# Kernel tuning notes

Hardware: AMD Instinct MI355X
Metric: run time of the kernel (lower is better)

Reference implementation:

```python
import jax, jax.numpy as jnp
import numpy as np

HEADS = 4
EPS = 1e-5


def _ln(x, g, b):
    m = jnp.mean(x, axis=-1, keepdims=True)
    v = jnp.mean((x - m) ** 2, axis=-1, keepdims=True)
    return (x - m) * jax.lax.rsqrt(v + EPS) * g + b


def _gcn(x, A, W, b):
    # x: [B,N,T,C]; A: [N,N]; W: [C_out, 3C] (1x1 conv); order-2 k-hop propagation
    h = jnp.transpose(x, (0, 3, 1, 2))            # [B,C,N,T]
    h1 = jnp.einsum('bcnt,nm->bcmt', h, A)        # 1-hop
    h2 = jnp.einsum('bcnt,nm->bcmt', h1, A)       # 2-hop
    cat = jnp.concatenate([h, h1, h2], axis=1)    # [B,3C,N,T]
    out = jnp.einsum('bcnt,oc->bont', cat, W) + b[None, :, None, None]
    return jnp.transpose(out, (0, 2, 3, 1))       # [B,N,T,C_out]


def setup_inputs() -> dict:
    key = jax.random.key(0)
    ks = jax.random.split(key, 16)
    B, N, T, H = 8, 2048, 1, 64
    s = 0.02
    return {
        'query': jax.random.normal(ks[0], (B, N, T, H), jnp.float32),
        'adj': jax.random.uniform(ks[1], (N, N), jnp.float32) / N,
        'WF': jax.random.normal(ks[2], (H, 3 * H), jnp.float32) * s,
        'bF': jnp.zeros((H,), jnp.float32),
        'WD': jax.random.normal(ks[3], (H, 3 * H), jnp.float32) * s,
        'bD': jnp.zeros((H,), jnp.float32),
        'ffw1': jax.random.normal(ks[4], (6 * H, H), jnp.float32) * s,
        'ffb1': jnp.zeros((6 * H,), jnp.float32),
        'ffw2': jax.random.normal(ks[5], (H, 6 * H), jnp.float32) * s,
        'ffb2': jnp.zeros((H,), jnp.float32),
        'wq': jax.random.normal(ks[6], (H, H), jnp.float32) * s,
        'wk': jax.random.normal(ks[7], (H, H), jnp.float32) * s,
        'wv': jax.random.normal(ks[8], (H, H), jnp.float32) * s,
        'wo': jax.random.normal(ks[9], (H, H), jnp.float32) * s,
        'bo': jnp.zeros((H,), jnp.float32),
        'g2': jnp.ones((H,), jnp.float32),
        'be2': jnp.zeros((H,), jnp.float32),
        'g3': jnp.ones((H,), jnp.float32),
        'be3': jnp.zeros((H,), jnp.float32),
        'f1w': jax.random.normal(ks[10], (4 * H, H), jnp.float32) * s,
        'f1b': jnp.zeros((4 * H,), jnp.float32),
        'f2w': jax.random.normal(ks[11], (H, 4 * H), jnp.float32) * s,
        'f2b': jnp.zeros((H,), jnp.float32),
    }


def reference(query, adj, WF, bF, WD, bD, ffw1, ffb1, ffw2, ffb2,
              wq, wk, wv, wo, bo, g2, be2, g3, be3, f1w, f1b, f2w, f2b):
    B, N, T, H = query.shape
    dh = H // HEADS
    # fixed-adjacency GCN branch
    X_F = _gcn(query, adj, WF, bF)
    # dynamic adjacency
    R = query.reshape(B, N, T * H)
    R = R @ ffw1.T + ffb1
    R = R @ ffw2.T + ffb2
    R = R.sum(axis=0)                              # [N,H]
    A = R @ R.T                                    # [N,N]
    Rm = jax.nn.relu(jax.nn.softmax(A, axis=-1)) + jnp.eye(N, dtype=A.dtype)
    X_D = _gcn(query, Rm, WD, bD)
    # gated fusion
    X_DF = jnp.tanh(X_D) * jax.nn.sigmoid(X_F)     # [B,N,T,H]
    # spatial multi-head attention over N
    def heads_split(x, w):
        return jnp.transpose((x @ w.T).reshape(B, N, T, HEADS, dh), (0, 3, 2, 1, 4))
    q = heads_split(X_DF, wq)                      # [B,h,T,N,dh]
    k = heads_split(X_DF, wk)
    v = heads_split(X_DF, wv)
    scores = jnp.einsum('bhtnd,bhtmd->bhtnm', q, k) / np.sqrt(dh)
    attn = jax.nn.softmax(scores, axis=-1)
    ctx = jnp.einsum('bhtnm,bhtmd->bhtnd', attn, v)
    ctx = jnp.transpose(ctx, (0, 3, 2, 1, 4)).reshape(B, N, T, H)
    att_out = ctx @ wo.T + bo
    x = _ln(att_out + X_DF, g2, be2)
    ffn = jax.nn.relu(x @ f1w.T + f1b) @ f2w.T + f2b
    return _ln(ffn + x, g3, be3)
```

## Files before the change

### kernel.cpp

```cpp
#include <hip/hip_runtime.h>
#include <math.h>

#define NN 2048
#define BB 8
#define HD 64

typedef __attribute__((ext_vector_type(8))) short bf16x8;
typedef __attribute__((ext_vector_type(4))) float f32x4;
typedef __attribute__((ext_vector_type(16))) float f32x16;
typedef __attribute__((ext_vector_type(4))) unsigned short ushortx4;
typedef unsigned short ushort_t;

static __device__ __forceinline__ float wsum64(float v) {
#pragma unroll
    for (int off = 32; off >= 1; off >>= 1) v += __shfl_xor(v, off);
    return v;
}
static __device__ __forceinline__ float wmax64(float v) {
#pragma unroll
    for (int off = 32; off >= 1; off >>= 1) v = fmaxf(v, __shfl_xor(v, off));
    return v;
}
static __device__ __forceinline__ unsigned short brne(float x) {
    unsigned u = __float_as_uint(x);
    return (unsigned short)((u + 0x7fffu + ((u >> 16) & 1u)) >> 16);
}

#define QSCL 0.36067376022224085f

__global__ void k_prep(const float* __restrict__ ffw1, const float* __restrict__ ffb1,
                       const float* __restrict__ ffw2, const float* __restrict__ ffb2,
                       const float* __restrict__ WF, const float* __restrict__ WD,
                       const float* __restrict__ wq, const float* __restrict__ wk,
                       const float* __restrict__ wv,
                       const float* __restrict__ f1w, const float* __restrict__ f2w,
                       float* __restrict__ Wc, float* __restrict__ bc,
                       ushort_t* __restrict__ Wfb, ushort_t* __restrict__ Wdb,
                       ushort_t* __restrict__ Wqkvb,
                       ushort_t* __restrict__ f1wb, ushort_t* __restrict__ f2wb) {
    int idx = blockIdx.x * 256 + threadIdx.x;
    if (idx < 4096) {
        int o = idx >> 6, c = idx & 63;
        float s = 0.f;
        for (int j = 0; j < 384; ++j) s += ffw2[o * 384 + j] * ffw1[j * 64 + c];
        Wc[idx] = s;
    }
    if (idx < 64) {
        float s = ffb2[idx];
        for (int j = 0; j < 384; ++j) s += ffw2[idx * 384 + j] * ffb1[j];
        bc[idx] = s;
    }
    if (idx < 12288) {
        Wfb[idx] = brne(WF[idx]);
        Wdb[idx] = brne(WD[idx]);
        int o = idx >> 6, c = idx & 63;
        float v = o < 64 ? wq[o * 64 + c] * QSCL
                         : (o < 128 ? wk[(o - 64) * 64 + c] : wv[(o - 128) * 64 + c]);
        Wqkvb[idx] = brne(v);
    }
    if (idx < 16384) {
        f1wb[idx] = brne(f1w[idx]);
        f2wb[idx] = brne(f2w[idx]);
    }
}

__global__ __launch_bounds__(256) void k_qprep(const float* __restrict__ q,
                                               float* __restrict__ Qcat,
                                               ushort_t* __restrict__ Qcatb,
                                               float* __restrict__ Qsum) {
    int idx = blockIdx.x * 256 + threadIdx.x;
    int n = idx >> 6, c = idx & 63;
    float s = 0.f;
#pragma unroll
    for (int b = 0; b < BB; ++b) {
        float v = q[((size_t)b * NN + n) * 64 + c];
        s += v;
        Qcat[(size_t)n * 512 + b * 64 + c] = v;
        Qcatb[(size_t)n * 512 + b * 64 + c] = brne(v);
    }
    Qsum[idx] = s;
}

__global__ __launch_bounds__(256) void k_rsum(const float* __restrict__ Qsum,
                                              const float* __restrict__ Wc,
                                              const float* __restrict__ bc,
                                              float* __restrict__ Rsum) {
    __shared__ float W[64][65];
    int tid = threadIdx.x;
    for (int i = tid; i < 4096; i += 256) W[i >> 6][i & 63] = Wc[i];
    __syncthreads();
    int idx = blockIdx.x * 256 + tid;
    int n = idx >> 6, h = idx & 63;
    const float* qs = &Qsum[n * 64];
    float s = 8.f * bc[h];
    for (int c = 0; c < 64; ++c) s += qs[c] * W[h][c];
    Rsum[idx] = s;
}

__global__ __launch_bounds__(256) void k_amat(const float* __restrict__ R, float* __restrict__ A) {
    __shared__ float Rn[64][65];
    __shared__ float Rm[64][65];
    int n0 = blockIdx.y * 64, m0 = blockIdx.x * 64;
    int tid = threadIdx.x;
    for (int i = tid; i < 4096; i += 256) {
        int r = i >> 6, c = i & 63;
        Rn[r][c] = R[(n0 + r) * 64 + c];
        Rm[r][c] = R[(m0 + r) * 64 + c];
    }
    __syncthreads();
    int tx = tid & 15, ty = tid >> 4;
    float acc[4][4] = {};
    for (int k = 0; k < 64; ++k) {
        float a[4], b[4];
#pragma unroll
        for (int i = 0; i < 4; ++i) a[i] = Rn[ty * 4 + i][k];
#pragma unroll
        for (int j = 0; j < 4; ++j) b[j] = Rm[tx * 4 + j][k];
#pragma unroll
        for (int i = 0; i < 4; ++i)
#pragma unroll
            for (int j = 0; j < 4; ++j) acc[i][j] += a[i] * b[j];
    }
#pragma unroll
    for (int i = 0; i < 4; ++i)
#pragma unroll
        for (int j = 0; j < 4; ++j)
            A[(size_t)(n0 + ty * 4 + i) * NN + m0 + tx * 4 + j] = acc[i][j];
}

__global__ __launch_bounds__(256) void k_softmax(float* __restrict__ A) {
    __shared__ float red[8];
    int n = blockIdx.x, tid = threadIdx.x;
    float4* row = (float4*)&A[(size_t)n * NN];
    float4 a = row[tid * 2], b = row[tid * 2 + 1];
    float v[8] = {a.x, a.y, a.z, a.w, b.x, b.y, b.z, b.w};
    float mx = v[0];
#pragma unroll
    for (int i = 1; i < 8; ++i) mx = fmaxf(mx, v[i]);
    mx = wmax64(mx);
    int wid = tid >> 6, lane = tid & 63;
    if (lane == 0) red[wid] = mx;
    __syncthreads();
    mx = fmaxf(fmaxf(red[0], red[1]), fmaxf(red[2], red[3]));
    float s = 0.f;
#pragma unroll
    for (int i = 0; i < 8; ++i) { v[i] = exp2f((v[i] - mx) * 1.44269504f); s += v[i]; }
    s = wsum64(s);
    if (lane == 0) red[4 + wid] = s;
    __syncthreads();
    s = red[4] + red[5] + red[6] + red[7];
    float inv = 1.f / s;
    int col = tid * 8;
#pragma unroll
    for (int i = 0; i < 8; ++i) v[i] = v[i] * inv + ((col + i) == n ? 1.f : 0.f);
    row[tid * 2]     = make_float4(v[0], v[1], v[2], v[3]);
    row[tid * 2 + 1] = make_float4(v[4], v[5], v[6], v[7]);
}

__global__ __launch_bounds__(256) void k_t32to16(const float* __restrict__ in,
                                                 ushort_t* __restrict__ out,
                                                 int R, int C) {
    __shared__ float tile[64][65];
    int r0 = blockIdx.y * 64, c0 = blockIdx.x * 64;
    int t = threadIdx.x;
    int tr = t >> 6, tc = t & 63;
#pragma unroll
    for (int i = 0; i < 16; ++i) {
        int r = tr + i * 4;
        tile[r][tc] = in[(size_t)(r0 + r) * C + c0 + tc];
    }
    __syncthreads();
#pragma unroll
    for (int i = 0; i < 16; ++i) {
        int cc = tr + i * 4;
        out[(size_t)(c0 + cc) * R + r0 + tc] = brne(tile[tc][cc]);
    }
}

__global__ __launch_bounds__(256) void k_hop(const ushort_t* __restrict__ G0t,
                                             const ushort_t* __restrict__ G1t,
                                             const ushort_t* __restrict__ B0t,
                                             const ushort_t* __restrict__ B1t,
                                             float* __restrict__ Y0, float* __restrict__ Y1,
                                             ushort_t* __restrict__ T0, ushort_t* __restrict__ T1,
                                             ushort_t* __restrict__ R0, ushort_t* __restrict__ R1) {
    __shared__ __align__(16) ushort_t As[4096];
    __shared__ __align__(16) ushort_t Bs[4096];
    int z = blockIdx.z;
    const ushort_t* Gt = z ? G1t : G0t;
    const ushort_t* Xt = z ? B1t : B0t;
    float* Y = z ? Y1 : Y0;
    ushort_t* T = z ? T1 : T0;
    ushort_t* R = z ? R1 : R0;
    int m0 = blockIdx.y * 64, j0 = blockIdx.x * 64;
    int t = threadIdx.x;
    int srow = t >> 2, scb = (t & 3) * 2;
    int sw = srow & 7;
    const int lane = t & 63, w = t >> 6;
    const int wm = w >> 1, wj = w & 1;
    const int lg = lane >> 4, lr = lane & 15;
    const int ma = wm * 32 + lr, mb = ma + 16;
    const int ja = wj * 32 + lr, jb = ja + 16;
    const int swa = ma & 7, swb = ja & 7;
    f32x4 acc00 = {}, acc01 = {}, acc10 = {}, acc11 = {};
    const size_t gbase = (size_t)(m0 + srow) * NN;
    const size_t xbase = (size_t)(j0 + srow) * NN;
    for (int k0 = 0; k0 < NN; k0 += 64) {
        bf16x8 g0 = *(const bf16x8*)(Gt + gbase + k0 + scb * 8);
        bf16x8 g1 = *(const bf16x8*)(Gt + gbase + k0 + scb * 8 + 8);
        bf16x8 x0 = *(const bf16x8*)(Xt + xbase + k0 + scb * 8);
        bf16x8 x1 = *(const bf16x8*)(Xt + xbase + k0 + scb * 8 + 8);
        __syncthreads();
        *(bf16x8*)&As[srow * 64 + ((scb    ) ^ sw) * 8] = g0;
        *(bf16x8*)&As[srow * 64 + ((scb + 1) ^ sw) * 8] = g1;
        *(bf16x8*)&Bs[srow * 64 + ((scb    ) ^ sw) * 8] = x0;
        *(bf16x8*)&Bs[srow * 64 + ((scb + 1) ^ sw) * 8] = x1;
        __syncthreads();
#pragma unroll
        for (int kk = 0; kk < 2; ++kk) {
            int c = kk * 4 + lg;
            bf16x8 a0 = *(const bf16x8*)&As[ma * 64 + (c ^ swa) * 8];
            bf16x8 a1 = *(const bf16x8*)&As[mb * 64 + (c ^ swa) * 8];
            bf16x8 b0 = *(const bf16x8*)&Bs[ja * 64 + (c ^ swb) * 8];
            bf16x8 b1 = *(const bf16x8*)&Bs[jb * 64 + (c ^ swb) * 8];
            acc00 = __builtin_amdgcn_mfma_f32_16x16x32_bf16(a0, b0, acc00, 0, 0, 0);
            acc01 = __builtin_amdgcn_mfma_f32_16x16x32_bf16(a0, b1, acc01, 0, 0, 0);
            acc10 = __builtin_amdgcn_mfma_f32_16x16x32_bf16(a1, b0, acc10, 0, 0, 0);
            acc11 = __builtin_amdgcn_mfma_f32_16x16x32_bf16(a1, b1, acc11, 0, 0, 0);
        }
    }
    int jA = j0 + wj * 32 + lr;
    int mA = m0 + wm * 32 + lg * 4;
    if (Y) {
#pragma unroll
        for (int r = 0; r < 4; ++r) {
            Y[(size_t)(mA + r) * 512 + jA]           = acc00[r];
            Y[(size_t)(mA + r) * 512 + jA + 16]      = acc01[r];
            Y[(size_t)(mA + 16 + r) * 512 + jA]      = acc10[r];
            Y[(size_t)(mA + 16 + r) * 512 + jA + 16] = acc11[r];
        }
    }
    if (T || R) {
        ushortx4 p0, p1, p2, p3;
#pragma unroll
        for (int r = 0; r < 4; ++r) {
            p0[r] = brne(acc00[r]);
            p1[r] = brne(acc01[r]);
            p2[r] = brne(acc10[r]);
            p3[r] = brne(acc11[r]);
        }
        if (T) {
            *(ushortx4*)&T[(size_t)jA * NN + mA]             = p0;
            *(ushortx4*)&T[(size_t)(jA + 16) * NN + mA]      = p1;
            *(ushortx4*)&T[(size_t)jA * NN + mA + 16]        = p2;
            *(ushortx4*)&T[(size_t)(jA + 16) * NN + mA + 16] = p3;
        }
        if (R) {
#pragma unroll
            for (int r = 0; r < 4; ++r) {
                R[(size_t)(mA + r) * 512 + jA]           = p0[r];
                R[(size_t)(mA + r) * 512 + jA + 16]      = p1[r];
                R[(size_t)(mA + 16 + r) * 512 + jA]      = p2[r];
                R[(size_t)(mA + 16 + r) * 512 + jA + 16] = p3[r];
            }
        }
    }
}

__global__ __launch_bounds__(256) void k_gcnz(const ushort_t* __restrict__ Qcatb,
                                              const ushort_t* __restrict__ X1Fb,
                                              const ushort_t* __restrict__ X2Fb,
                                              const ushort_t* __restrict__ X1Db,
                                              const ushort_t* __restrict__ X2Db,
                                              const ushort_t* __restrict__ Wfb,
                                              const ushort_t* __restrict__ Wdb,
                                              const float* __restrict__ bF,
                                              const float* __restrict__ bD,
                                              float* __restrict__ XDF,
                                              ushort_t* __restrict__ XDFb) {
    __shared__ ushort_t Wl[2][64][200];
    int tid = threadIdx.x;
    for (int i = tid; i < 12288; i += 256) {
        int o = i / 192, k = i % 192;
        Wl[0][o][k] = Wfb[i];
        Wl[1][o][k] = Wdb[i];
    }
    int blk = blockIdx.x;
    int b = blk >> 5, n0 = (blk & 31) * 64;
    int lane = tid & 63, rt = tid >> 6;
    int lr = lane & 15, lg = lane >> 4;
    int nA = n0 + rt * 16 + lr;
    const size_t rb = (size_t)nA * 512 + b * 64 + lg * 8;
    bf16x8 aQ0  = *(const bf16x8*)(Qcatb + rb);
    bf16x8 aQ1  = *(const bf16x8*)(Qcatb + rb + 32);
    bf16x8 a1F0 = *(const bf16x8*)(X1Fb + rb);
    bf16x8 a1F1 = *(const bf16x8*)(X1Fb + rb + 32);
    bf16x8 a2F0 = *(const bf16x8*)(X2Fb + rb);
    bf16x8 a2F1 = *(const bf16x8*)(X2Fb + rb + 32);
    bf16x8 a1D0 = *(const bf16x8*)(X1Db + rb);
    bf16x8 a1D1 = *(const bf16x8*)(X1Db + rb + 32);
    bf16x8 a2D0 = *(const bf16x8*)(X2Db + rb);
    bf16x8 a2D1 = *(const bf16x8*)(X2Db + rb + 32);
    float bFv[4], bDv[4];
#pragma unroll
    for (int ot = 0; ot < 4; ++ot) { bFv[ot] = bF[ot * 16 + lr]; bDv[ot] = bD[ot * 16 + lr]; }
    __syncthreads();
    f32x4 accF[4], accD[4];
#pragma unroll
    for (int ot = 0; ot < 4; ++ot) {
        int o = ot * 16 + lr;
        const ushort_t* wf = &Wl[0][o][lg * 8];
        const ushort_t* wd = &Wl[1][o][lg * 8];
        f32x4 aF = {}, aD = {};
        aF = __builtin_amdgcn_mfma_f32_16x16x32_bf16(aQ0,  *(const bf16x8*)(wf),       aF, 0, 0, 0);
        aF = __builtin_amdgcn_mfma_f32_16x16x32_bf16(aQ1,  *(const bf16x8*)(wf + 32),  aF, 0, 0, 0);
        aF = __builtin_amdgcn_mfma_f32_16x16x32_bf16(a1F0, *(const bf16x8*)(wf + 64),  aF, 0, 0, 0);
        aF = __builtin_amdgcn_mfma_f32_16x16x32_bf16(a1F1, *(const bf16x8*)(wf + 96),  aF, 0, 0, 0);
        aF = __builtin_amdgcn_mfma_f32_16x16x32_bf16(a2F0, *(const bf16x8*)(wf + 128), aF, 0, 0, 0);
        aF = __builtin_amdgcn_mfma_f32_16x16x32_bf16(a2F1, *(const bf16x8*)(wf + 160), aF, 0, 0, 0);
        aD = __builtin_amdgcn_mfma_f32_16x16x32_bf16(aQ0,  *(const bf16x8*)(wd),       aD, 0, 0, 0);
        aD = __builtin_amdgcn_mfma_f32_16x16x32_bf16(aQ1,  *(const bf16x8*)(wd + 32),  aD, 0, 0, 0);
        aD = __builtin_amdgcn_mfma_f32_16x16x32_bf16(a1D0, *(const bf16x8*)(wd + 64),  aD, 0, 0, 0);
        aD = __builtin_amdgcn_mfma_f32_16x16x32_bf16(a1D1, *(const bf16x8*)(wd + 96),  aD, 0, 0, 0);
        aD = __builtin_amdgcn_mfma_f32_16x16x32_bf16(a2D0, *(const bf16x8*)(wd + 128), aD, 0, 0, 0);
        aD = __builtin_amdgcn_mfma_f32_16x16x32_bf16(a2D1, *(const bf16x8*)(wd + 160), aD, 0, 0, 0);
        accF[ot] = aF; accD[ot] = aD;
    }
    const float L2E = 1.44269504f;
#pragma unroll
    for (int ot = 0; ot < 4; ++ot) {
#pragma unroll
        for (int r = 0; r < 4; ++r) {
            float f = accF[ot][r] + bFv[ot];
            float d = accD[ot][r] + bDv[ot];
            float sg = 1.f / (1.f + exp2f(-f * L2E));
            float th = 2.f / (1.f + exp2f(-2.f * d * L2E)) - 1.f;
            float xv = th * sg;
            int nD = n0 + rt * 16 + lg * 4 + r;
            size_t oa = ((size_t)b * NN + nD) * 64 + ot * 16 + lr;
            XDF[oa] = xv;
            XDFb[oa] = brne(xv);
        }
    }
}

__global__ __launch_bounds__(256) void k_qkvm(const ushort_t* __restrict__ XDFb,
                                              const ushort_t* __restrict__ Wqkvb,
                                              ushort_t* __restrict__ qb,
                                              ushort_t* __restrict__ kb,
                                              ushort_t* __restrict__ vbt) {
    __shared__ ushort_t Wl[192][72];
    __shared__ float vt[4][64][17];
    int tid = threadIdx.x;
    for (int i = tid; i < 12288; i += 256) Wl[i >> 6][i & 63] = Wqkvb[i];
    int blk = blockIdx.x;
    size_t row0 = (size_t)blk * 64;
    int b = (int)(row0 >> 11), nbase = (int)(row0 & 2047);
    int lane = tid & 63, rt = tid >> 6;
    int lr = lane & 15, lg = lane >> 4;
    int nl = rt * 16 + lr;
    const ushort_t* xr = XDFb + (row0 + nl) * 64 + lg * 8;
    bf16x8 a0 = *(const bf16x8*)(xr);
    bf16x8 a1 = *(const bf16x8*)(xr + 32);
    __syncthreads();
#pragma unroll
    for (int ot = 0; ot < 12; ++ot) {
        f32x4 acc = {};
        const ushort_t* wp = &Wl[ot * 16 + lr][lg * 8];
        acc = __builtin_amdgcn_mfma_f32_16x16x32_bf16(a0, *(const bf16x8*)(wp),      acc, 0, 0, 0);
        acc = __builtin_amdgcn_mfma_f32_16x16x32_bf16(a1, *(const bf16x8*)(wp + 32), acc, 0, 0, 0);
        int kind = ot >> 2, h = ot & 3;
        int nD = rt * 16 + lg * 4;
        if (kind < 2) {
            ushort_t* dst = (kind == 0 ? qb : kb) + (((size_t)(b * 4 + h) * NN + nbase + nD) * 16 + lr);
#pragma unroll
            for (int r = 0; r < 4; ++r) dst[r * 16] = brne(acc[r]);
        } else {
#pragma unroll
            for (int r = 0; r < 4; ++r) vt[h][nD + r][lr] = acc[r];
        }
    }
    __syncthreads();
    if (tid < 128) {
        int h = tid >> 5, d = (tid >> 1) & 15, half = tid & 1;
        ushort_t* dst = vbt + ((size_t)(b * 4 + h) * 32 + d) * NN + nbase + half * 32;
#pragma unroll
        for (int g = 0; g < 4; ++g) {
            uint4 u;
            int i0 = half * 32 + g * 8;
            u.x = (unsigned)brne(vt[h][i0 + 0][d]) | ((unsigned)brne(vt[h][i0 + 1][d]) << 16);
            u.y = (unsigned)brne(vt[h][i0 + 2][d]) | ((unsigned)brne(vt[h][i0 + 3][d]) << 16);
            u.z = (unsigned)brne(vt[h][i0 + 4][d]) | ((unsigned)brne(vt[h][i0 + 5][d]) << 16);
            u.w = (unsigned)brne(vt[h][i0 + 6][d]) | ((unsigned)brne(vt[h][i0 + 7][d]) << 16);
            ((uint4*)dst)[g] = u;
        }
    } else {
        int t2 = tid - 128;
        int h = t2 >> 5, dz = 16 + ((t2 >> 1) & 15), half = t2 & 1;
        unsigned pv = (dz == 16) ? 0x3F803F80u : 0u;
        uint4 z; z.x = pv; z.y = pv; z.z = pv; z.w = pv;
        ushort_t* dst = vbt + ((size_t)(b * 4 + h) * 32 + dz) * NN + nbase + half * 32;
#pragma unroll
        for (int g = 0; g < 4; ++g) ((uint4*)dst)[g] = z;
    }
}

__global__ __launch_bounds__(256) void k_attn_mf(const ushort_t* __restrict__ qb,
                                                 const ushort_t* __restrict__ kb,
                                                 const ushort_t* __restrict__ vbt,
                                                 float* __restrict__ ctx) {
    __shared__ float cpart[4][32][33];
    int bh = blockIdx.y, n0 = blockIdx.x * 64;
    int tid = threadIdx.x, w = tid >> 6, l = tid & 63;
    int lc = l & 31, hi = l >> 5;
    int qsub = w & 1, mhalf = w >> 1;
    const ushort_t* Q  = qb + ((size_t)bh * NN + n0 + qsub * 32) * 16;
    const ushort_t* K  = kb + (size_t)bh * NN * 16;
    const ushort_t* VT = vbt + ((size_t)bh * 32 + lc) * NN;
    bf16x8 qf = *(const bf16x8*)(Q + lc * 16 + hi * 8);
    f32x16 zero = {};
    f32x16 acc = {};
    for (int m0 = mhalf * 32; m0 < NN; m0 += 64) {
        bf16x8 kf = *(const bf16x8*)(K + (size_t)(m0 + lc) * 16 + hi * 8);
        bf16x8 v0 = *(const bf16x8*)(VT + m0 + hi * 8);
        bf16x8 v1 = *(const bf16x8*)(VT + m0 + 16 + hi * 8);
        f32x16 st = __builtin_amdgcn_mfma_f32_32x32x16_bf16(kf, qf, zero, 0, 0, 0);
        float p[16];
#pragma unroll
        for (int r = 0; r < 16; ++r) p[r] = exp2f(st[r]);
        unsigned d[8];
#pragma unroll
        for (int j = 0; j < 8; ++j)
            asm("v_cvt_pk_bf16_f32 %0, %1, %2" : "=v"(d[j]) : "v"(p[2 * j]), "v"(p[2 * j + 1]));
        unsigned s[8];
#pragma unroll
        for (int j = 0; j < 8; ++j) s[j] = (unsigned)__shfl_xor((int)d[j], 32);
        union { bf16x8 v; unsigned u[4]; } fa, fb;
        if (hi == 0) {
            fa.u[0] = d[0]; fa.u[1] = d[1]; fa.u[2] = s[0]; fa.u[3] = s[1];
            fb.u[0] = d[4]; fb.u[1] = d[5]; fb.u[2] = s[4]; fb.u[3] = s[5];
        } else {
            fa.u[0] = s[2]; fa.u[1] = s[3]; fa.u[2] = d[2]; fa.u[3] = d[3];
            fb.u[0] = s[6]; fb.u[1] = s[7]; fb.u[2] = d[6]; fb.u[3] = d[7];
        }
        acc = __builtin_amdgcn_mfma_f32_32x32x16_bf16(fa.v, v0, acc, 0, 0, 0);
        acc = __builtin_amdgcn_mfma_f32_32x32x16_bf16(fb.v, v1, acc, 0, 0, 0);
    }
#pragma unroll
    for (int r = 0; r < 16; ++r)
        cpart[w][(r & 3) + 8 * (r >> 2) + 4 * hi][lc] = acc[r];
    __syncthreads();
    int q = tid >> 2, d4 = (tid & 3) * 4;
    int qs = q >> 5, q32 = q & 31;
    float sst = cpart[qs][q32][16] + cpart[2 + qs][q32][16];
    float inv = 1.f / sst;
    float4 o;
    o.x = (cpart[qs][q32][d4]     + cpart[2 + qs][q32][d4])     * inv;
    o.y = (cpart[qs][q32][d4 + 1] + cpart[2 + qs][q32][d4 + 1]) * inv;
    o.z = (cpart[qs][q32][d4 + 2] + cpart[2 + qs][q32][d4 + 2]) * inv;
    o.w = (cpart[qs][q32][d4 + 3] + cpart[2 + qs][q32][d4 + 3]) * inv;
    int b = bh >> 2, h = bh & 3;
    *(float4*)&ctx[((size_t)b * NN + n0 + q) * 64 + h * 16 + d4] = o;
}

__global__ __launch_bounds__(256) void k_post1(const float* __restrict__ ctx,
                                               const float* __restrict__ XDF,
                                               const float* __restrict__ wo,
                                               const float* __restrict__ bo,
                                               const float* __restrict__ g2,
                                               const float* __restrict__ be2,
                                               float* __restrict__ xout) {
    __shared__ float W[64][65];
    __shared__ float xs[4][64];
    int tid = threadIdx.x;
    for (int i = tid; i < 4096; i += 256) W[i >> 6][i & 63] = wo[i];
    int row0 = blockIdx.x * 4;
    xs[tid >> 6][tid & 63] = ctx[(size_t)row0 * 64 + tid];
    __syncthreads();
    int r = tid >> 6, o = tid & 63;
    int row = row0 + r;
    const float* x = xs[r];
    float y = bo[o];
    for (int c = 0; c < 64; ++c) y += x[c] * W[o][c];
    y += XDF[(size_t)row * 64 + o];
    float mean = wsum64(y) * (1.f / 64.f);
    float d = y - mean;
    float var = wsum64(d * d) * (1.f / 64.f);
    float rstd = rsqrtf(var + 1e-5f);
    xout[(size_t)row * 64 + o] = d * rstd * g2[o] + be2[o];
}

__global__ __launch_bounds__(256) void k_ffn(const float* __restrict__ x,
                                             const ushort_t* __restrict__ f1wb,
                                             const float* __restrict__ f1b,
                                             const ushort_t* __restrict__ f2wb,
                                             const float* __restrict__ f2b,
                                             const float* __restrict__ g3,
                                             const float* __restrict__ be3,
                                             float* __restrict__ out) {
    __shared__ ushort_t xs[64][72];
    __shared__ ushort_t tl[64][264];
    int tid = threadIdx.x;
    size_t row0 = (size_t)blockIdx.x * 64;
    for (int i = tid; i < 1024; i += 256) {
        int r = i >> 4, c4 = (i & 15) * 4;
        float4 v = *(const float4*)&x[(row0 + r) * 64 + c4];
        xs[r][c4] = brne(v.x); xs[r][c4 + 1] = brne(v.y);
        xs[r][c4 + 2] = brne(v.z); xs[r][c4 + 3] = brne(v.w);
    }
    __syncthreads();
    int lane = tid & 63, rt = tid >> 6;
    int lr = lane & 15, lg = lane >> 4;
    bf16x8 a0 = *(const bf16x8*)&xs[rt * 16 + lr][lg * 8];
    bf16x8 a1 = *(const bf16x8*)&xs[rt * 16 + lr][32 + lg * 8];
#pragma unroll
    for (int jt = 0; jt < 16; ++jt) {
        f32x4 acc = {};
        const ushort_t* wp = f1wb + (size_t)(jt * 16 + lr) * 64 + lg * 8;
        acc = __builtin_amdgcn_mfma_f32_16x16x32_bf16(a0, *(const bf16x8*)(wp),      acc, 0, 0, 0);
        acc = __builtin_amdgcn_mfma_f32_16x16x32_bf16(a1, *(const bf16x8*)(wp + 32), acc, 0, 0, 0);
        float bj = f1b[jt * 16 + lr];
#pragma unroll
        for (int r = 0; r < 4; ++r)
            tl[rt * 16 + lg * 4 + r][jt * 16 + lr] = brne(fmaxf(acc[r] + bj, 0.f));
    }
    __syncthreads();
    bf16x8 af[8];
#pragma unroll
    for (int kc = 0; kc < 8; ++kc)
        af[kc] = *(const bf16x8*)&tl[rt * 16 + lr][kc * 32 + lg * 8];
    f32x4 acc2[4];
#pragma unroll
    for (int ot = 0; ot < 4; ++ot) {
        f32x4 a = {};
#pragma unroll
        for (int kc = 0; kc < 8; ++kc) {
            bf16x8 bf = *(const bf16x8*)(f2wb + (size_t)(ot * 16 + lr) * 256 + kc * 32 + lg * 8);
            a = __builtin_amdgcn_mfma_f32_16x16x32_bf16(af[kc], bf, a, 0, 0, 0);
        }
        acc2[ot] = a;
    }
    float g3v[4], be3v[4], f2bv[4];
#pragma unroll
    for (int ot = 0; ot < 4; ++ot) {
        int o = ot * 16 + lr;
        g3v[ot] = g3[o]; be3v[ot] = be3[o]; f2bv[ot] = f2b[o];
    }
#pragma unroll
    for (int r = 0; r < 4; ++r) {
        int rowL = rt * 16 + lg * 4 + r;
        float y[4]; float s = 0.f;
#pragma unroll
        for (int ot = 0; ot < 4; ++ot) {
            y[ot] = acc2[ot][r] + f2bv[ot] + x[(row0 + rowL) * 64 + ot * 16 + lr];
            s += y[ot];
        }
        s += __shfl_xor(s, 1); s += __shfl_xor(s, 2);
        s += __shfl_xor(s, 4); s += __shfl_xor(s, 8);
        float mean = s * (1.f / 64.f);
        float vs = 0.f;
#pragma unroll
        for (int ot = 0; ot < 4; ++ot) { float dd = y[ot] - mean; vs += dd * dd; }
        vs += __shfl_xor(vs, 1); vs += __shfl_xor(vs, 2);
        vs += __shfl_xor(vs, 4); vs += __shfl_xor(vs, 8);
        float rstd = rsqrtf(vs * (1.f / 64.f) + 1e-5f);
#pragma unroll
        for (int ot = 0; ot < 4; ++ot)
            out[(row0 + rowL) * 64 + ot * 16 + lr] = (y[ot] - mean) * rstd * g3v[ot] + be3v[ot];
    }
}

extern "C" void kernel_launch(void* const* d_in, const int* in_sizes, int n_in,
                              void* d_out, int out_size, void* d_ws, size_t ws_size,
                              hipStream_t stream) {
    const float* query = (const float*)d_in[0];
    const float* adj   = (const float*)d_in[1];
    const float* WF    = (const float*)d_in[2];
    const float* bF    = (const float*)d_in[3];
    const float* WD    = (const float*)d_in[4];
    const float* bD    = (const float*)d_in[5];
    const float* ffw1  = (const float*)d_in[6];
    const float* ffb1  = (const float*)d_in[7];
    const float* ffw2  = (const float*)d_in[8];
    const float* ffb2  = (const float*)d_in[9];
    const float* wq    = (const float*)d_in[10];
    const float* wk    = (const float*)d_in[11];
    const float* wv    = (const float*)d_in[12];
    const float* wo    = (const float*)d_in[13];
    const float* bo    = (const float*)d_in[14];
    const float* g2    = (const float*)d_in[15];
    const float* be2   = (const float*)d_in[16];
    const float* g3    = (const float*)d_in[17];
    const float* be3   = (const float*)d_in[18];
    const float* f1w   = (const float*)d_in[19];
    const float* f1b   = (const float*)d_in[20];
    const float* f2w   = (const float*)d_in[21];
    const float* f2b   = (const float*)d_in[22];
    float* out = (float*)d_out;

    float* w = (float*)d_ws;
    float*    Qcat  = w;
    float*    Qsum  = w + 1048576;
    float*    Wc    = w + 1179648;
    float*    bc    = w + 1183744;
    ushort_t* Wfb   = (ushort_t*)(w + 1184000);
    ushort_t* Wdb   = (ushort_t*)(w + 1190144);
    ushort_t* Wqkvb = (ushort_t*)(w + 1196288);
    ushort_t* f1wb  = (ushort_t*)(w + 1202432);
    ushort_t* f2wb  = (ushort_t*)(w + 1210624);
    float*    Rsum  = w + 1218816;
    float*    Amat  = w + 1349888;
    ushort_t* adjT  = (ushort_t*)(w + 5544192);
    ushort_t* RmT   = (ushort_t*)(w + 7641344);
    ushort_t* QcatT = (ushort_t*)(w + 9738496);
    ushort_t* Qcatb = (ushort_t*)(w + 10262784);
    ushort_t* X1FT  = (ushort_t*)(w + 10787072);
    ushort_t* X1DT  = (ushort_t*)(w + 11311360);
    ushort_t* X1Fb  = (ushort_t*)(w + 11835648);
    ushort_t* X1Db  = (ushort_t*)(w + 12359936);
    ushort_t* X2Db  = (ushort_t*)(w + 12884224);
    ushort_t* X2Fb  = QcatT;
    ushort_t* qb    = (ushort_t*)Qcat;
    ushort_t* kb    = (ushort_t*)(Qcat + 524288);
    ushort_t* vbt   = (ushort_t*)Amat;
    float*    ctxb  = Amat + 1048576;
    float*    XDF   = (float*)adjT;
    float*    x1    = (float*)adjT + 1048576;
    ushort_t* XDFb  = RmT;

    k_prep<<<64, 256, 0, stream>>>(ffw1, ffb1, ffw2, ffb2, WF, WD, wq, wk, wv, f1w, f2w,
                                   Wc, bc, Wfb, Wdb, Wqkvb, f1wb, f2wb);
    k_qprep<<<512, 256, 0, stream>>>(query, Qcat, Qcatb, Qsum);
    k_rsum<<<512, 256, 0, stream>>>(Qsum, Wc, bc, Rsum);
    k_amat<<<dim3(32, 32), 256, 0, stream>>>(Rsum, Amat);
    k_softmax<<<2048, 256, 0, stream>>>(Amat);

    k_t32to16<<<dim3(32, 32), 256, 0, stream>>>(adj, adjT, NN, NN);
    k_t32to16<<<dim3(32, 32), 256, 0, stream>>>(Amat, RmT, NN, NN);
    k_t32to16<<<dim3(8, 32), 256, 0, stream>>>(Qcat, QcatT, NN, 512);

    k_hop<<<dim3(8, 32, 2), 256, 0, stream>>>(adjT, RmT, QcatT, QcatT,
                                              nullptr, nullptr, X1FT, X1DT, X1Fb, X1Db);
    k_hop<<<dim3(8, 32, 2), 256, 0, stream>>>(adjT, RmT, X1FT, X1DT,
                                              nullptr, nullptr, nullptr, nullptr, X2Fb, X2Db);

    k_gcnz<<<256, 256, 0, stream>>>(Qcatb, X1Fb, X2Fb, X1Db, X2Db, Wfb, Wdb, bF, bD,
                                    XDF, XDFb);
    k_qkvm<<<256, 256, 0, stream>>>(XDFb, Wqkvb, qb, kb, vbt);
    k_attn_mf<<<dim3(32, 32), 256, 0, stream>>>(qb, kb, vbt, ctxb);
    k_post1<<<4096, 256, 0, stream>>>(ctxb, XDF, wo, bo, g2, be2, x1);
    k_ffn<<<256, 256, 0, stream>>>(x1, f1wb, f1b, f2wb, f2b, g3, be3, out);
}
```

Measured before the change: 315.9 us.

## Use MFMA for R·Rᵀ, fuse output projection+LN into FFN, halve attention shuffles

Replaces the scalar fp32 A=R·Rᵀ kernel with a bf16 MFMA version that reads a bf16 R and uses swizzled LDS. It fuses the attention output projection and first LayerNorm into the FFN kernel, with ctx now stored as bf16 and wo converted to bf16 in prep. This removes a kernel launch and the fp32 x1 round trip. The attention loop now does four cross-half shuffles instead of eight. Computing the softmax logits and ctx in bf16 adds rounding error in exchange.

```diff
diff --git a/kernel.cpp b/kernel.cpp
--- a/kernel.cpp
+++ b/kernel.cpp
@@ -32,11 +32,11 @@
                        const float* __restrict__ ffw2, const float* __restrict__ ffb2,
                        const float* __restrict__ WF, const float* __restrict__ WD,
                        const float* __restrict__ wq, const float* __restrict__ wk,
-                       const float* __restrict__ wv,
+                       const float* __restrict__ wv, const float* __restrict__ wo,
                        const float* __restrict__ f1w, const float* __restrict__ f2w,
                        float* __restrict__ Wc, float* __restrict__ bc,
                        ushort_t* __restrict__ Wfb, ushort_t* __restrict__ Wdb,
-                       ushort_t* __restrict__ Wqkvb,
+                       ushort_t* __restrict__ Wqkvb, ushort_t* __restrict__ wob,
                        ushort_t* __restrict__ f1wb, ushort_t* __restrict__ f2wb) {
     int idx = blockIdx.x * 256 + threadIdx.x;
     if (idx < 4096) {
@@ -44,6 +44,7 @@
         float s = 0.f;
         for (int j = 0; j < 384; ++j) s += ffw2[o * 384 + j] * ffw1[j * 64 + c];
         Wc[idx] = s;
+        wob[idx] = brne(wo[idx]);
     }
     if (idx < 64) {
         float s = ffb2[idx];
@@ -84,7 +85,7 @@
 __global__ __launch_bounds__(256) void k_rsum(const float* __restrict__ Qsum,
                                               const float* __restrict__ Wc,
                                               const float* __restrict__ bc,
-                                              float* __restrict__ Rsum) {
+                                              ushort_t* __restrict__ Rsumb) {
     __shared__ float W[64][65];
     int tid = threadIdx.x;
     for (int i = tid; i < 4096; i += 256) W[i >> 6][i & 63] = Wc[i];
@@ -94,38 +95,54 @@
     const float* qs = &Qsum[n * 64];
     float s = 8.f * bc[h];
     for (int c = 0; c < 64; ++c) s += qs[c] * W[h][c];
-    Rsum[idx] = s;
-}
-
-__global__ __launch_bounds__(256) void k_amat(const float* __restrict__ R, float* __restrict__ A) {
-    __shared__ float Rn[64][65];
-    __shared__ float Rm[64][65];
+    Rsumb[idx] = brne(s);
+}
+
+__global__ __launch_bounds__(256) void k_amat_m(const ushort_t* __restrict__ Rb,
+                                                float* __restrict__ A) {
+    __shared__ __align__(16) ushort_t As[4096];
+    __shared__ __align__(16) ushort_t Bs[4096];
     int n0 = blockIdx.y * 64, m0 = blockIdx.x * 64;
-    int tid = threadIdx.x;
-    for (int i = tid; i < 4096; i += 256) {
-        int r = i >> 6, c = i & 63;
-        Rn[r][c] = R[(n0 + r) * 64 + c];
-        Rm[r][c] = R[(m0 + r) * 64 + c];
-    }
-    __syncthreads();
-    int tx = tid & 15, ty = tid >> 4;
-    float acc[4][4] = {};
-    for (int k = 0; k < 64; ++k) {
-        float a[4], b[4];
-#pragma unroll
-        for (int i = 0; i < 4; ++i) a[i] = Rn[ty * 4 + i][k];
-#pragma unroll
-        for (int j = 0; j < 4; ++j) b[j] = Rm[tx * 4 + j][k];
-#pragma unroll
-        for (int i = 0; i < 4; ++i)
-#pragma unroll
-            for (int j = 0; j < 4; ++j) acc[i][j] += a[i] * b[j];
-    }
-#pragma unroll
-    for (int i = 0; i < 4; ++i)
-#pragma unroll
-        for (int j = 0; j < 4; ++j)
-            A[(size_t)(n0 + ty * 4 + i) * NN + m0 + tx * 4 + j] = acc[i][j];
+    int t = threadIdx.x;
+    int srow = t >> 2, scb = (t & 3) * 2;
+    int sw = srow & 7;
+    const int lane = t & 63, w = t >> 6;
+    const int wm = w >> 1, wj = w & 1;
+    const int lg = lane >> 4, lr = lane & 15;
+    const int ma = wm * 32 + lr, mb = ma + 16;
+    const int ja = wj * 32 + lr, jb = ja + 16;
+    const int swa = ma & 7, swb = ja & 7;
+    bf16x8 g0 = *(const bf16x8*)(Rb + (size_t)(n0 + srow) * 64 + scb * 8);
+    bf16x8 g1 = *(const bf16x8*)(Rb + (size_t)(n0 + srow) * 64 + scb * 8 + 8);
+    bf16x8 x0 = *(const bf16x8*)(Rb + (size_t)(m0 + srow) * 64 + scb * 8);
+    bf16x8 x1 = *(const bf16x8*)(Rb + (size_t)(m0 + srow) * 64 + scb * 8 + 8);
+    *(bf16x8*)&As[srow * 64 + ((scb    ) ^ sw) * 8] = g0;
+    *(bf16x8*)&As[srow * 64 + ((scb + 1) ^ sw) * 8] = g1;
+    *(bf16x8*)&Bs[srow * 64 + ((scb    ) ^ sw) * 8] = x0;
+    *(bf16x8*)&Bs[srow * 64 + ((scb + 1) ^ sw) * 8] = x1;
+    __syncthreads();
+    f32x4 acc00 = {}, acc01 = {}, acc10 = {}, acc11 = {};
+#pragma unroll
+    for (int kk = 0; kk < 2; ++kk) {
+        int c = kk * 4 + lg;
+        bf16x8 a0 = *(const bf16x8*)&As[ma * 64 + (c ^ swa) * 8];
+        bf16x8 a1 = *(const bf16x8*)&As[mb * 64 + (c ^ swa) * 8];
+        bf16x8 b0 = *(const bf16x8*)&Bs[ja * 64 + (c ^ swb) * 8];
+        bf16x8 b1 = *(const bf16x8*)&Bs[jb * 64 + (c ^ swb) * 8];
+        acc00 = __builtin_amdgcn_mfma_f32_16x16x32_bf16(a0, b0, acc00, 0, 0, 0);
+        acc01 = __builtin_amdgcn_mfma_f32_16x16x32_bf16(a0, b1, acc01, 0, 0, 0);
+        acc10 = __builtin_amdgcn_mfma_f32_16x16x32_bf16(a1, b0, acc10, 0, 0, 0);
+        acc11 = __builtin_amdgcn_mfma_f32_16x16x32_bf16(a1, b1, acc11, 0, 0, 0);
+    }
+    int jA = m0 + wj * 32 + lr;
+    int nA = n0 + wm * 32 + lg * 4;
+#pragma unroll
+    for (int r = 0; r < 4; ++r) {
+        A[(size_t)(nA + r) * NN + jA]           = acc00[r];
+        A[(size_t)(nA + r) * NN + jA + 16]      = acc01[r];
+        A[(size_t)(nA + 16 + r) * NN + jA]      = acc10[r];
+        A[(size_t)(nA + 16 + r) * NN + jA + 16] = acc11[r];
+    }
 }
 
 __global__ __launch_bounds__(256) void k_softmax(float* __restrict__ A) {
@@ -408,7 +425,7 @@
 __global__ __launch_bounds__(256) void k_attn_mf(const ushort_t* __restrict__ qb,
                                                  const ushort_t* __restrict__ kb,
                                                  const ushort_t* __restrict__ vbt,
-                                                 float* __restrict__ ctx) {
+                                                 ushort_t* __restrict__ ctx) {
     __shared__ float cpart[4][32][33];
     int bh = blockIdx.y, n0 = blockIdx.x * 64;
     int tid = threadIdx.x, w = tid >> 6, l = tid & 63;
@@ -432,16 +449,21 @@
 #pragma unroll
         for (int j = 0; j < 8; ++j)
             asm("v_cvt_pk_bf16_f32 %0, %1, %2" : "=v"(d[j]) : "v"(p[2 * j]), "v"(p[2 * j + 1]));
-        unsigned s[8];
-#pragma unroll
-        for (int j = 0; j < 8; ++j) s[j] = (unsigned)__shfl_xor((int)d[j], 32);
+        unsigned z0 = hi ? d[0] : d[2];
+        unsigned z1 = hi ? d[1] : d[3];
+        unsigned z2 = hi ? d[4] : d[6];
+        unsigned z3 = hi ? d[5] : d[7];
+        unsigned r0 = (unsigned)__shfl_xor((int)z0, 32);
+        unsigned r1 = (unsigned)__shfl_xor((int)z1, 32);
+        unsigned r2 = (unsigned)__shfl_xor((int)z2, 32);
+        unsigned r3 = (unsigned)__shfl_xor((int)z3, 32);
         union { bf16x8 v; unsigned u[4]; } fa, fb;
         if (hi == 0) {
-            fa.u[0] = d[0]; fa.u[1] = d[1]; fa.u[2] = s[0]; fa.u[3] = s[1];
-            fb.u[0] = d[4]; fb.u[1] = d[5]; fb.u[2] = s[4]; fb.u[3] = s[5];
+            fa.u[0] = d[0]; fa.u[1] = d[1]; fa.u[2] = r0; fa.u[3] = r1;
+            fb.u[0] = d[4]; fb.u[1] = d[5]; fb.u[2] = r2; fb.u[3] = r3;
         } else {
-            fa.u[0] = s[2]; fa.u[1] = s[3]; fa.u[2] = d[2]; fa.u[3] = d[3];
-            fb.u[0] = s[6]; fb.u[1] = s[7]; fb.u[2] = d[6]; fb.u[3] = d[7];
+            fa.u[0] = r0; fa.u[1] = r1; fa.u[2] = d[2]; fa.u[3] = d[3];
+            fb.u[0] = r2; fb.u[1] = r3; fb.u[2] = d[6]; fb.u[3] = d[7];
         }
         acc = __builtin_amdgcn_mfma_f32_32x32x16_bf16(fa.v, v0, acc, 0, 0, 0);
         acc = __builtin_amdgcn_mfma_f32_32x32x16_bf16(fb.v, v1, acc, 0, 0, 0);
@@ -454,63 +476,79 @@
     int qs = q >> 5, q32 = q & 31;
     float sst = cpart[qs][q32][16] + cpart[2 + qs][q32][16];
     float inv = 1.f / sst;
-    float4 o;
-    o.x = (cpart[qs][q32][d4]     + cpart[2 + qs][q32][d4])     * inv;
-    o.y = (cpart[qs][q32][d4 + 1] + cpart[2 + qs][q32][d4 + 1]) * inv;
-    o.z = (cpart[qs][q32][d4 + 2] + cpart[2 + qs][q32][d4 + 2]) * inv;
-    o.w = (cpart[qs][q32][d4 + 3] + cpart[2 + qs][q32][d4 + 3]) * inv;
+    ushortx4 ob;
+    ob[0] = brne((cpart[qs][q32][d4]     + cpart[2 + qs][q32][d4])     * inv);
+    ob[1] = brne((cpart[qs][q32][d4 + 1] + cpart[2 + qs][q32][d4 + 1]) * inv);
+    ob[2] = brne((cpart[qs][q32][d4 + 2] + cpart[2 + qs][q32][d4 + 2]) * inv);
+    ob[3] = brne((cpart[qs][q32][d4 + 3] + cpart[2 + qs][q32][d4 + 3]) * inv);
     int b = bh >> 2, h = bh & 3;
-    *(float4*)&ctx[((size_t)b * NN + n0 + q) * 64 + h * 16 + d4] = o;
-}
-
-__global__ __launch_bounds__(256) void k_post1(const float* __restrict__ ctx,
-                                               const float* __restrict__ XDF,
-                                               const float* __restrict__ wo,
-                                               const float* __restrict__ bo,
-                                               const float* __restrict__ g2,
-                                               const float* __restrict__ be2,
-                                               float* __restrict__ xout) {
-    __shared__ float W[64][65];
-    __shared__ float xs[4][64];
-    int tid = threadIdx.x;
-    for (int i = tid; i < 4096; i += 256) W[i >> 6][i & 63] = wo[i];
-    int row0 = blockIdx.x * 4;
-    xs[tid >> 6][tid & 63] = ctx[(size_t)row0 * 64 + tid];
-    __syncthreads();
-    int r = tid >> 6, o = tid & 63;
-    int row = row0 + r;
-    const float* x = xs[r];
-    float y = bo[o];
-    for (int c = 0; c < 64; ++c) y += x[c] * W[o][c];
-    y += XDF[(size_t)row * 64 + o];
-    float mean = wsum64(y) * (1.f / 64.f);
-    float d = y - mean;
-    float var = wsum64(d * d) * (1.f / 64.f);
-    float rstd = rsqrtf(var + 1e-5f);
-    xout[(size_t)row * 64 + o] = d * rstd * g2[o] + be2[o];
-}
-
-__global__ __launch_bounds__(256) void k_ffn(const float* __restrict__ x,
-                                             const ushort_t* __restrict__ f1wb,
-                                             const float* __restrict__ f1b,
-                                             const ushort_t* __restrict__ f2wb,
-                                             const float* __restrict__ f2b,
-                                             const float* __restrict__ g3,
-                                             const float* __restrict__ be3,
-                                             float* __restrict__ out) {
+    *(ushortx4*)&ctx[((size_t)b * NN + n0 + q) * 64 + h * 16 + d4] = ob;
+}
+
+__global__ __launch_bounds__(256) void k_tail(const ushort_t* __restrict__ ctxb,
+                                              const float* __restrict__ XDF,
+                                              const ushort_t* __restrict__ wob,
+                                              const float* __restrict__ bo,
+                                              const float* __restrict__ g2,
+                                              const float* __restrict__ be2,
+                                              const ushort_t* __restrict__ f1wb,
+                                              const float* __restrict__ f1b,
+                                              const ushort_t* __restrict__ f2wb,
+                                              const float* __restrict__ f2b,
+                                              const float* __restrict__ g3,
+                                              const float* __restrict__ be3,
+                                              float* __restrict__ out) {
     __shared__ ushort_t xs[64][72];
     __shared__ ushort_t tl[64][264];
     int tid = threadIdx.x;
     size_t row0 = (size_t)blockIdx.x * 64;
-    for (int i = tid; i < 1024; i += 256) {
-        int r = i >> 4, c4 = (i & 15) * 4;
-        float4 v = *(const float4*)&x[(row0 + r) * 64 + c4];
-        xs[r][c4] = brne(v.x); xs[r][c4 + 1] = brne(v.y);
-        xs[r][c4 + 2] = brne(v.z); xs[r][c4 + 3] = brne(v.w);
-    }
-    __syncthreads();
     int lane = tid & 63, rt = tid >> 6;
     int lr = lane & 15, lg = lane >> 4;
+    const ushort_t* cr = ctxb + (row0 + rt * 16 + lr) * 64 + lg * 8;
+    bf16x8 c0 = *(const bf16x8*)(cr);
+    bf16x8 c1 = *(const bf16x8*)(cr + 32);
+    f32x4 acc1[4];
+#pragma unroll
+    for (int ot = 0; ot < 4; ++ot) {
+        f32x4 a = {};
+        const ushort_t* wp = wob + (size_t)(ot * 16 + lr) * 64 + lg * 8;
+        a = __builtin_amdgcn_mfma_f32_16x16x32_bf16(c0, *(const bf16x8*)(wp),      a, 0, 0, 0);
+        a = __builtin_amdgcn_mfma_f32_16x16x32_bf16(c1, *(const bf16x8*)(wp + 32), a, 0, 0, 0);
+        acc1[ot] = a;
+    }
+    float bov[4], g2v[4], be2v[4];
+#pragma unroll
+    for (int ot = 0; ot < 4; ++ot) {
+        int ch = ot * 16 + lr;
+        bov[ot] = bo[ch]; g2v[ot] = g2[ch]; be2v[ot] = be2[ch];
+    }
+    float x1k[4][4];
+#pragma unroll
+    for (int r = 0; r < 4; ++r) {
+        int rowL = rt * 16 + lg * 4 + r;
+        float y[4]; float s = 0.f;
+#pragma unroll
+        for (int ot = 0; ot < 4; ++ot) {
+            y[ot] = acc1[ot][r] + bov[ot] + XDF[(row0 + rowL) * 64 + ot * 16 + lr];
+            s += y[ot];
+        }
+        s += __shfl_xor(s, 1); s += __shfl_xor(s, 2);
+        s += __shfl_xor(s, 4); s += __shfl_xor(s, 8);
+        float mean = s * (1.f / 64.f);
+        float vs = 0.f;
+#pragma unroll
+        for (int ot = 0; ot < 4; ++ot) { float dd = y[ot] - mean; vs += dd * dd; }
+        vs += __shfl_xor(vs, 1); vs += __shfl_xor(vs, 2);
+        vs += __shfl_xor(vs, 4); vs += __shfl_xor(vs, 8);
+        float rstd = rsqrtf(vs * (1.f / 64.f) + 1e-5f);
+#pragma unroll
+        for (int ot = 0; ot < 4; ++ot) {
+            float v = (y[ot] - mean) * rstd * g2v[ot] + be2v[ot];
+            x1k[r][ot] = v;
+            xs[rowL][ot * 16 + lr] = brne(v);
+        }
+    }
+    __syncthreads();
     bf16x8 a0 = *(const bf16x8*)&xs[rt * 16 + lr][lg * 8];
     bf16x8 a1 = *(const bf16x8*)&xs[rt * 16 + lr][32 + lg * 8];
 #pragma unroll
@@ -552,7 +590,7 @@
         float y[4]; float s = 0.f;
 #pragma unroll
         for (int ot = 0; ot < 4; ++ot) {
-            y[ot] = acc2[ot][r] + f2bv[ot] + x[(row0 + rowL) * 64 + ot * 16 + lr];
+            y[ot] = acc2[ot][r] + f2bv[ot] + x1k[r][ot];
             s += y[ot];
         }
         s += __shfl_xor(s, 1); s += __shfl_xor(s, 2);
@@ -608,7 +646,8 @@
     ushort_t* Wqkvb = (ushort_t*)(w + 1196288);
     ushort_t* f1wb  = (ushort_t*)(w + 1202432);
     ushort_t* f2wb  = (ushort_t*)(w + 1210624);
-    float*    Rsum  = w + 1218816;
+    ushort_t* Rsumb = (ushort_t*)(w + 1218816);
+    ushort_t* wob   = (ushort_t*)(w + 1284352);
     float*    Amat  = w + 1349888;
     ushort_t* adjT  = (ushort_t*)(w + 5544192);
     ushort_t* RmT   = (ushort_t*)(w + 7641344);
@@ -623,16 +662,15 @@
     ushort_t* qb    = (ushort_t*)Qcat;
     ushort_t* kb    = (ushort_t*)(Qcat + 524288);
     ushort_t* vbt   = (ushort_t*)Amat;
-    float*    ctxb  = Amat + 1048576;
+    ushort_t* ctxb  = (ushort_t*)(Amat + 1048576);
     float*    XDF   = (float*)adjT;
-    float*    x1    = (float*)adjT + 1048576;
     ushort_t* XDFb  = RmT;
 
-    k_prep<<<64, 256, 0, stream>>>(ffw1, ffb1, ffw2, ffb2, WF, WD, wq, wk, wv, f1w, f2w,
-                                   Wc, bc, Wfb, Wdb, Wqkvb, f1wb, f2wb);
+    k_prep<<<64, 256, 0, stream>>>(ffw1, ffb1, ffw2, ffb2, WF, WD, wq, wk, wv, wo, f1w, f2w,
+                                   Wc, bc, Wfb, Wdb, Wqkvb, wob, f1wb, f2wb);
     k_qprep<<<512, 256, 0, stream>>>(query, Qcat, Qcatb, Qsum);
-    k_rsum<<<512, 256, 0, stream>>>(Qsum, Wc, bc, Rsum);
-    k_amat<<<dim3(32, 32), 256, 0, stream>>>(Rsum, Amat);
+    k_rsum<<<512, 256, 0, stream>>>(Qsum, Wc, bc, Rsumb);
+    k_amat_m<<<dim3(32, 32), 256, 0, stream>>>(Rsumb, Amat);
     k_softmax<<<2048, 256, 0, stream>>>(Amat);
 
     k_t32to16<<<dim3(32, 32), 256, 0, stream>>>(adj, adjT, NN, NN);
@@ -648,6 +686,6 @@
                                     XDF, XDFb);
     k_qkvm<<<256, 256, 0, stream>>>(XDFb, Wqkvb, qb, kb, vbt);
     k_attn_mf<<<dim3(32, 32), 256, 0, stream>>>(qb, kb, vbt, ctxb);
-    k_post1<<<4096, 256, 0, stream>>>(ctxb, XDF, wo, bo, g2, be2, x1);
-    k_ffn<<<256, 256, 0, stream>>>(x1, f1wb, f1b, f2wb, f2b, g3, be3, out);
-}
+    k_tail<<<256, 256, 0, stream>>>(ctxb, XDF, wob, bo, g2, be2,
+                                    f1wb, f1b, f2wb, f2b, g3, be3, out);
+}
```

Result: faster. 292.3 us (-7.5%).
